# Optimization experiments

Hardware: AMD Instinct MI355X
Metric: run time of the kernel (lower is better)

The kernel has to match this reference:

```python
import jax, jax.numpy as jnp
import numpy as np
from jax import lax

EMB, HID, L, PATCH, IMG, K = 192, 64, 6, 4, 224, 8
FMAP = IMG // PATCH
N = FMAP * FMAP
B = 8
ALG = 4
GB_np = np.array([0, 1, 1, 2])  # grade of each blade [1, e1, e2, e12]
GB = jnp.asarray(GB_np)

def _cayley_np():
    C = np.zeros((4, 4, 4), np.float32)
    tbl = {(0,0):(0,1.),(0,1):(1,1.),(0,2):(2,1.),(0,3):(3,1.),
           (1,0):(1,1.),(1,1):(0,1.),(1,2):(3,1.),(1,3):(2,1.),
           (2,0):(2,1.),(2,1):(3,-1.),(2,2):(0,1.),(2,3):(1,-1.),
           (3,0):(3,1.),(3,1):(2,-1.),(3,2):(1,1.),(3,3):(0,-1.)}
    for (i, j), (k, s) in tbl.items():
        C[i, j, k] = s
    return C

CAY_np = _cayley_np()
CAYLEY = jnp.asarray(CAY_np)
_paths = np.zeros((3, 3, 3), bool)
for _i in range(4):
    for _j in range(4):
        for _k in range(4):
            if CAY_np[_i, _j, _k] != 0:
                _paths[GB_np[_i], GB_np[_j], GB_np[_k]] = True
PI, PJ, PK = (jnp.asarray(a) for a in np.nonzero(_paths))
NPATH = int(_paths.sum())  # 10 geometric-product paths for Cl(2,0)

def build_knn_graph(H, W, k):
    yy, xx = np.meshgrid(np.arange(H, dtype=np.float32), np.arange(W, dtype=np.float32), indexing='ij')
    coords = np.stack([xx.ravel(), yy.ravel()], -1)
    cn = coords / np.array([W - 1, H - 1], np.float32) * 2 - 1
    d = np.linalg.norm(cn[:, None] - cn[None], axis=-1)
    np.fill_diagonal(d, np.inf)
    idx = np.argsort(d, axis=-1, kind='stable')[:, :k]
    rows = np.repeat(np.arange(H * W), k)
    cols = idx.reshape(-1)
    return rows.astype(np.int32), cols.astype(np.int32), cn.astype(np.float32)

def mvlin(x, W, b=None):
    # per-grade MVLinear: W [out,in,3] expanded to blades via GB
    y = jnp.einsum('nmi,bmi->bni', W[:, :, GB], x)
    if b is not None:
        y = y.at[:, :, 0].add(b)  # bias embedded in scalar blade only
    return y

def mvlin_flat(x, W, b):
    # subspaces=False MVLinear: same weight across blades
    y = jnp.einsum('nm,bmi->bni', W, x)
    return y.at[:, :, 0].add(b)

def mv_silu(x, a, b):
    # invariants: [scalar, q(grade1), q(grade2)]; gate = sigmoid(a*inv+b)
    inv = jnp.concatenate([x[..., :1], x[..., 1:2]**2 + x[..., 2:3]**2, x[..., 3:4]**2], -1)
    return jax.nn.sigmoid(a * inv + b)[..., GB] * x

def normalize_mv(x, a):
    q = jnp.concatenate([x[..., :1]**2, x[..., 1:2]**2 + x[..., 2:3]**2, x[..., 3:4]**2], -1)
    n = jnp.sqrt(q + 1e-12)
    d = jax.nn.sigmoid(a) * (n - 1.0) + 1.0
    return x / (d + 1e-6)[..., GB]

def sgp(x, Wl, bl, Wr, na, gw):
    # SteerableGeometricProductLayer
    xr = normalize_mv(mvlin(x, Wr), na)
    full = jnp.zeros((gw.shape[0], 3, 3, 3), x.dtype).at[:, PI, PJ, PK].set(gw)
    fb = full[:, GB][:, :, GB][:, :, :, GB]  # [feat,4,4,4]
    gp = jnp.einsum('bni,nijk,bnk->bnj', x, CAYLEY[None] * fb, xr)
    return (mvlin(x, Wl, bl) + gp) * np.float32(1.0 / np.sqrt(2.0))

def _forward(x, conv_w, conv_b, stem_g, stem_b, pos_embed, in_W, in_b, in_Wl, in_bl, in_Wr, in_na, in_gw, eg_eW, eg_eb, eg_sa, eg_sb, eg_nW, eg_nb, eg_Wl, eg_bl, eg_Wr, eg_na, eg_gw, eg_aa, eg_ab, out_W, out_b, on_g, on_b, cls_W, cls_b, coords, rows, cols):
    Bx = x.shape[0]
    # stem: strided conv + LayerNorm over (C,H,W)
    y = lax.conv_general_dilated(x, conv_w, (PATCH, PATCH), 'VALID', dimension_numbers=('NCHW', 'OIHW', 'NCHW')) + conv_b[None, :, None, None]
    mu = y.mean(axis=(1, 2, 3), keepdims=True)
    var = ((y - mu) ** 2).mean(axis=(1, 2, 3), keepdims=True)
    y = (y - mu) / jnp.sqrt(var + 1e-5) * stem_g[None] + stem_b[None]
    y = y + pos_embed
    feat = y.transpose(0, 2, 3, 1).reshape(Bx * N, EMB)
    # embed features in scalar blade, coordinates in vector blades e1,e2
    h = jnp.zeros((Bx * N, EMB + 1, ALG), x.dtype)
    h = h.at[:, :EMB, 0].set(feat)
    h = h.at[:, EMB, 1:3].set(jnp.tile(coords, (Bx, 1)))
    h = sgp(mvlin_flat(h, in_W, in_b), in_Wl, in_bl, in_Wr, in_na, in_gw)
    BN = Bx * N
    for i in range(L):
        m = mv_silu(mvlin(h[rows] - h[cols], eg_eW[i], eg_eb[i]), eg_sa[i], eg_sb[i])
        agg = jax.ops.segment_sum(m, rows, num_segments=BN)  # count computed but unused in original
        nu = mvlin(jnp.concatenate([h, agg], axis=1), eg_nW[i], eg_nb[i])
        out = mv_silu(sgp(nu, eg_Wl[i], eg_bl[i], eg_Wr[i], eg_na[i], eg_gw[i]), eg_aa[i], eg_ab[i])
        h = h + out if i > 0 else out
    s = mvlin_flat(h, out_W, out_b)[..., 0]
    mu2 = s.mean(-1, keepdims=True)
    v2 = ((s - mu2) ** 2).mean(-1, keepdims=True)
    s = (s - mu2) / jnp.sqrt(v2 + 1e-5) * on_g + on_b
    pooled = s.reshape(Bx, N, EMB).mean(axis=1)
    return pooled @ cls_W.T + cls_b

def setup_inputs() -> dict:
    key = jax.random.key(0)
    ks = iter(jax.random.split(key, 64))
    nrm = lambda shape, s=0.05: jax.random.normal(next(ks), shape, jnp.float32) * s
    rows, cols, cn = build_knn_graph(FMAP, FMAP, K)
    offs = np.arange(B, dtype=np.int32)[:, None] * N
    rows_b = (rows[None] + offs).reshape(-1)
    cols_b = (cols[None] + offs).reshape(-1)
    return dict(
        x=jax.random.normal(next(ks), (B, 3, IMG, IMG), jnp.float32),
        conv_w=nrm((EMB, 3, PATCH, PATCH)),
        conv_b=jnp.zeros((EMB,), jnp.float32),
        stem_g=jnp.ones((EMB, FMAP, FMAP), jnp.float32),
        stem_b=jnp.zeros((EMB, FMAP, FMAP), jnp.float32),
        pos_embed=nrm((1, EMB, FMAP, FMAP), 0.02),
        coords=jnp.asarray(cn),
        in_W=nrm((HID, EMB + 1)), in_b=jnp.zeros((HID,), jnp.float32),
        in_Wl=nrm((HID, HID, 3)), in_bl=jnp.zeros((HID,), jnp.float32),
        in_Wr=nrm((HID, HID, 3)), in_na=jnp.zeros((HID, 3), jnp.float32),
        in_gw=nrm((HID, NPATH), 0.2),
        eg_eW=nrm((L, HID, HID, 3)), eg_eb=jnp.zeros((L, HID), jnp.float32),
        eg_sa=jnp.ones((L, HID, 3), jnp.float32), eg_sb=jnp.zeros((L, HID, 3), jnp.float32),
        eg_nW=nrm((L, HID, 2 * HID, 3)), eg_nb=jnp.zeros((L, HID), jnp.float32),
        eg_Wl=nrm((L, HID, HID, 3)), eg_bl=jnp.zeros((L, HID), jnp.float32),
        eg_Wr=nrm((L, HID, HID, 3)), eg_na=jnp.zeros((L, HID, 3), jnp.float32),
        eg_gw=nrm((L, HID, NPATH), 0.2),
        eg_aa=jnp.ones((L, HID, 3), jnp.float32), eg_ab=jnp.zeros((L, HID, 3), jnp.float32),
        out_W=nrm((EMB, HID)), out_b=jnp.zeros((EMB,), jnp.float32),
        on_g=jnp.ones((EMB,), jnp.float32), on_b=jnp.zeros((EMB,), jnp.float32),
        cls_W=nrm((10, EMB), 0.02), cls_b=jnp.zeros((10,), jnp.float32),
        rows=jnp.asarray(rows_b), cols=jnp.asarray(cols_b),
    )

def reference(x, conv_w, conv_b, stem_g, stem_b, pos_embed, coords, in_W, in_b, in_Wl, in_bl, in_Wr, in_na, in_gw, eg_eW, eg_eb, eg_sa, eg_sb, eg_nW, eg_nb, eg_Wl, eg_bl, eg_Wr, eg_na, eg_gw, eg_aa, eg_ab, out_W, out_b, on_g, on_b, cls_W, cls_b, rows, cols):
    return _forward(x, conv_w, conv_b, stem_g, stem_b, pos_embed, in_W, in_b, in_Wl, in_bl, in_Wr, in_na, in_gw, eg_eW, eg_eb, eg_sa, eg_sb, eg_nW, eg_nb, eg_Wl, eg_bl, eg_Wr, eg_na, eg_gw, eg_aa, eg_ab, out_W, out_b, on_g, on_b, cls_W, cls_b, coords, rows, cols)
```

## Files before the change

### kernel.cpp

```cpp
#include <hip/hip_runtime.h>
#include <hip/hip_bf16.h>
#include <math.h>

#define EMBC   192
#define NLAY   6
#define IMGC   224
#define FMAPC  56
#define NNODE  3136
#define NBATCH 8
#define BNODES 25088
#define KNNE   8
#define NT     64
#define RSQRT2 0.70710678118654752f

__device__ __forceinline__ float sigm(float x){ return 1.0f/(1.0f+__expf(-x)); }

__global__ void k_repackw(const float* __restrict__ src, float* __restrict__ dst, int K){
  int l = blockIdx.y;
  size_t S = (size_t)64*K*3;
  int t = blockIdx.x*256 + threadIdx.x;
  if(t < (int)S){
    int j = t % 3; int r = t / 3;
    int ci = r % 8; int m = (r / 8) % K; int wid = r / (8*K);
    dst[l*S + (((size_t)wid*K + m)*8 + ci)*3 + j] =
      src[l*S + ((size_t)(wid*8+ci)*K + m)*3 + j];
  }
}
__global__ void k_repack1(const float* __restrict__ src, float* __restrict__ dst,
                          int R, int K){
  int t = blockIdx.x*256 + threadIdx.x;
  if(t < R*K){
    int m = t % K, r = t / K;
    dst[m*R + r] = src[r*K + m];
  }
}

__global__ void k_tr(const float* __restrict__ g, const float* __restrict__ sb,
                     const float* __restrict__ pe, float* __restrict__ g2,
                     float* __restrict__ pb2){
  int n = blockIdx.x; int c = threadIdx.x;
  g2[n*EMBC + c]  = g[c*NNODE + n];
  pb2[n*EMBC + c] = sb[c*NNODE + n] + pe[c*NNODE + n];
}

__global__ __launch_bounds__(256) void k_conv(const float* __restrict__ x,
    const float* __restrict__ cw, const float* __restrict__ cb,
    float* __restrict__ y0, float* __restrict__ parts){
  __shared__ float xs[2688];
  __shared__ float wsh[9216];
  __shared__ float red[512];
  int blk = blockIdx.x; int b = blk / FMAPC; int ph = blk % FMAPC;
  int tid = threadIdx.x;
  for(int t = tid; t < 9216; t += 256) wsh[t] = cw[t];
  for(int t = tid; t < 2688; t += 256){
    int r = t / IMGC; int w = t % IMGC;
    int ci = r >> 2, kh = r & 3;
    xs[t] = x[((size_t)(b*3 + ci)*IMGC + (ph*4 + kh))*IMGC + w];
  }
  __syncthreads();
  float s1 = 0.f, s2 = 0.f;
  for(int oi = tid; oi < FMAPC*EMBC; oi += 256){
    int pw = oi / EMBC; int c = oi % EMBC;
    float acc = cb[c];
    const float4* wv4 = (const float4*)(wsh + c*48);
    #pragma unroll
    for(int r = 0; r < 12; ++r){
      float4 xv = *((const float4*)(xs + r*IMGC + pw*4));
      float4 wv = wv4[r];
      acc += xv.x*wv.x + xv.y*wv.y + xv.z*wv.z + xv.w*wv.w;
    }
    y0[((size_t)(b*NNODE + ph*FMAPC + pw))*EMBC + c] = acc;
    s1 += acc; s2 += acc*acc;
  }
  red[tid] = s1; red[256+tid] = s2;
  __syncthreads();
  for(int st = 128; st > 0; st >>= 1){
    if(tid < st){ red[tid] += red[tid+st]; red[256+tid] += red[256+tid+st]; }
    __syncthreads();
  }
  if(tid == 0){ parts[blk*2] = red[0]; parts[blk*2+1] = red[256]; }
}

__global__ void k_stats(const float* __restrict__ parts, float* __restrict__ stats){
  int b = threadIdx.x;
  if(b < NBATCH){
    float S = 0.f, Q = 0.f;
    for(int j = 0; j < FMAPC; ++j){ S += parts[(b*FMAPC+j)*2]; Q += parts[(b*FMAPC+j)*2+1]; }
    float cnt = (float)(EMBC*NNODE);
    float mu = S/cnt;
    float var = Q/cnt - mu*mu;
    stats[b*2] = mu; stats[b*2+1] = rsqrtf(var + 1e-5f);
  }
}

__global__ __launch_bounds__(256,2) void k_embed(const float* __restrict__ y0,
    const float* __restrict__ stats, const float* __restrict__ g2,
    const float* __restrict__ pb2, const float* __restrict__ inWp,
    const float* __restrict__ inb, const float* __restrict__ coords,
    float* __restrict__ xmv){
  __shared__ float fs[64*193];
  int tid = threadIdx.x, lane = tid & 63;
  int wid = __builtin_amdgcn_readfirstlane(tid >> 6);
  int ch0 = wid << 4;
  int p0 = blockIdx.x * 64;
  int b = p0 / NNODE; int n0 = p0 - b*NNODE;
  float mu = stats[b*2], rstd = stats[b*2+1];
  for(int t = tid; t < 64*192; t += 256){
    int n = t / 192, c = t - n*192;
    int nn = n0 + n;
    fs[n*193 + c] = (y0[(size_t)(p0+n)*192 + c] - mu)*rstd*g2[nn*192+c] + pb2[nn*192+c];
  }
  __syncthreads();
  float acc[16];
  #pragma unroll
  for(int ci = 0; ci < 16; ++ci) acc[ci] = 0.f;
  #pragma unroll 2
  for(int m = 0; m < 192; ++m){
    float xm = fs[lane*193 + m];
    const float* wp = inWp + m*64 + ch0;
    #pragma unroll
    for(int ci = 0; ci < 16; ++ci) acc[ci] += wp[ci]*xm;
  }
  float cx = coords[(n0+lane)*2], cy = coords[(n0+lane)*2+1];
  #pragma unroll
  for(int ci = 0; ci < 16; ++ci){
    int ch = ch0 + ci;
    float wc = inWp[192*64 + ch];
    float4 v; v.x = acc[ci] + inb[ch]; v.y = wc*cx; v.z = wc*cy; v.w = 0.f;
    *((float4*)(xmv + ((size_t)(p0+lane)*64 + ch)*4)) = v;
  }
}

__device__ __forceinline__ void stage_x(float* xs, const float* __restrict__ g,
                                        int p0, int tid){
  #pragma unroll
  for(int t = tid; t < NT*64; t += 512){
    int n = t >> 6, m = t & 63;
    *((float4*)(xs + (n<<8) + (((m + n)&63)<<2))) =
      *((const float4*)(g + (((size_t)(p0+n))<<8) + (m<<2)));
  }
}
__device__ __forceinline__ void copyout(const float* xs, float* __restrict__ g,
                                        int p0, int tid){
  #pragma unroll
  for(int t = tid; t < NT*64; t += 512){
    int n = t >> 6, m = t & 63;
    float4 v = *((const float4*)(xs + (n<<8) + (((m + n)&63)<<2)));
    *((float4*)(g + (((size_t)(p0+n))<<8) + (m<<2))) = v;
  }
}
__device__ __forceinline__ void stage_w(float* wst, const float* __restrict__ Wp,
                                        int K, int moff, int tid){
  #pragma unroll
  for(int t = tid; t < 3072; t += 512){
    int c = t / 384, r = t - c*384;
    ((float4*)wst)[t] = ((const float4*)(Wp + ((size_t)(c*K + moff)*24)))[r];
  }
}
__device__ __forceinline__ void mm2(float (&p)[4][4], float (&q)[4][4],
    const float* __restrict__ wst, const float* __restrict__ xr0,
    const float* __restrict__ xr1, int wb, int n){
  #pragma unroll 4
  for(int m = 0; m < 64; ++m){
    float4 x0 = *((const float4*)(xr0 + (((m + n)&63)<<2)));
    float4 x1 = *((const float4*)(xr1 + (((m + n + 32)&63)<<2)));
    const float* wp = wst + wb + m*24;
    float4 a = *((const float4*)wp);
    float4 b = *((const float4*)(wp+4));
    float4 c = *((const float4*)(wp+8));
    p[0][0]+=a.x*x0.x; p[0][1]+=a.y*x0.y; p[0][2]+=a.y*x0.z; p[0][3]+=a.z*x0.w;
    p[1][0]+=a.w*x0.x; p[1][1]+=b.x*x0.y; p[1][2]+=b.x*x0.z; p[1][3]+=b.y*x0.w;
    p[2][0]+=b.z*x0.x; p[2][1]+=b.w*x0.y; p[2][2]+=b.w*x0.z; p[2][3]+=c.x*x0.w;
    p[3][0]+=c.y*x0.x; p[3][1]+=c.z*x0.y; p[3][2]+=c.z*x0.z; p[3][3]+=c.w*x0.w;
    q[0][0]+=a.x*x1.x; q[0][1]+=a.y*x1.y; q[0][2]+=a.y*x1.z; q[0][3]+=a.z*x1.w;
    q[1][0]+=a.w*x1.x; q[1][1]+=b.x*x1.y; q[1][2]+=b.x*x1.z; q[1][3]+=b.y*x1.w;
    q[2][0]+=b.z*x1.x; q[2][1]+=b.w*x1.y; q[2][2]+=b.w*x1.z; q[2][3]+=c.x*x1.w;
    q[3][0]+=c.y*x1.x; q[3][1]+=c.z*x1.y; q[3][2]+=c.z*x1.z; q[3][3]+=c.w*x1.w;
  }
}
#define ZERO44(A) { _Pragma("unroll") for(int _i=0;_i<4;++_i) _Pragma("unroll") for(int _j=0;_j<4;++_j) A[_i][_j]=0.f; }

__global__ __launch_bounds__(512,1) void k_sgp0(const float* __restrict__ src,
    float* __restrict__ h, float* __restrict__ zout,
    const float* __restrict__ Wlp, const float* __restrict__ bl,
    const float* __restrict__ Wrp, const float* __restrict__ na,
    const float* __restrict__ gw, const float* __restrict__ zWp){
  __shared__ float xs[NT*256];
  __shared__ float wst[12288];
  int tid = threadIdx.x, lane = tid & 63;
  int wid = __builtin_amdgcn_readfirstlane(tid >> 6);
  int n = lane & 31, s = lane >> 5;
  int ch0 = (wid<<3) + s*4;
  int wb = wid*1536 + s*12;
  int p0 = blockIdx.x * NT;
  const float* xr0 = xs + (n<<8);
  const float* xr1 = xs + ((n+32)<<8);
  stage_x(xs, src, p0, tid);
  stage_w(wst, Wlp, 64, 0, tid);
  __syncthreads();
  float lA[4][4], lB[4][4], rA[4][4], rB[4][4];
  ZERO44(lA); ZERO44(lB); ZERO44(rA); ZERO44(rB);
  mm2(lA, lB, wst, xr0, xr1, wb, n);
  __syncthreads();
  stage_w(wst, Wrp, 64, 0, tid);
  __syncthreads();
  mm2(rA, rB, wst, xr0, xr1, wb, n);
  float oA[4][4], oB[4][4];
  #pragma unroll
  for(int j = 0; j < 2; ++j){
    int nn = n + j*32;
    #pragma unroll
    for(int ci = 0; ci < 4; ++ci){
      int ch = ch0 + ci;
      float yr0 = j? rB[ci][0]:rA[ci][0], yr1 = j? rB[ci][1]:rA[ci][1];
      float yr2 = j? rB[ci][2]:rA[ci][2], yr3 = j? rB[ci][3]:rA[ci][3];
      float na0 = sigm(na[ch*3]), na1 = sigm(na[ch*3+1]), na2 = sigm(na[ch*3+2]);
      float d0 = na0*(sqrtf(yr0*yr0 + 1e-12f) - 1.f) + 1.f + 1e-6f;
      float d1 = na1*(sqrtf(yr1*yr1 + yr2*yr2 + 1e-12f) - 1.f) + 1.f + 1e-6f;
      float d2 = na2*(sqrtf(yr3*yr3 + 1e-12f) - 1.f) + 1.f + 1e-6f;
      float xq0 = yr0/d0, xq1 = yr1/d1, xq2 = yr2/d1, xq3 = yr3/d2;
      float4 xv = *((const float4*)(xs + (nn<<8) + (((ch + nn)&63)<<2)));
      const float* gwp = gw + ch*10;
      float gp0 = gwp[0]*xv.x*xq0 + gwp[3]*(xv.y*xq1 + xv.z*xq2) + gwp[7]*xv.w*xq3;
      float gp1 = gwp[1]*xv.x*xq1 + gwp[4]*xv.y*xq0 - gwp[5]*xv.z*xq3 - gwp[8]*xv.w*xq2;
      float gp2 = gwp[1]*xv.x*xq2 + gwp[4]*xv.z*xq0 + gwp[5]*xv.y*xq3 + gwp[8]*xv.w*xq1;
      float gp3 = gwp[2]*xv.x*xq3 + gwp[6]*(xv.y*xq2 - xv.z*xq1) - gwp[9]*xv.w*xq0;
      float l0 = j? lB[ci][0]:lA[ci][0], l1 = j? lB[ci][1]:lA[ci][1];
      float l2 = j? lB[ci][2]:lA[ci][2], l3 = j? lB[ci][3]:lA[ci][3];
      float* o = j? oB[ci] : oA[ci];
      o[0] = (l0 + bl[ch] + gp0)*RSQRT2;
      o[1] = (l1 + gp1)*RSQRT2;
      o[2] = (l2 + gp2)*RSQRT2;
      o[3] = (l3 + gp3)*RSQRT2;
    }
  }
  __syncthreads();
  #pragma unroll
  for(int ci = 0; ci < 4; ++ci){
    int ch = ch0 + ci;
    float4 v0; v0.x=oA[ci][0]; v0.y=oA[ci][1]; v0.z=oA[ci][2]; v0.w=oA[ci][3];
    *((float4*)(xs + (n<<8) + (((ch + n)&63)<<2))) = v0;
    float4 v1; v1.x=oB[ci][0]; v1.y=oB[ci][1]; v1.z=oB[ci][2]; v1.w=oB[ci][3];
    *((float4*)(xs + ((n+32)<<8) + (((ch + n + 32)&63)<<2))) = v1;
  }
  __syncthreads();
  copyout(xs, h, p0, tid);
  stage_w(wst, zWp, 64, 0, tid);
  __syncthreads();
  float zA[4][4], zB[4][4];
  ZERO44(zA); ZERO44(zB);
  mm2(zA, zB, wst, xr0, xr1, wb, n);
  __syncthreads();
  #pragma unroll
  for(int ci = 0; ci < 4; ++ci){
    int ch = ch0 + ci;
    float4 v0; v0.x=zA[ci][0]; v0.y=zA[ci][1]; v0.z=zA[ci][2]; v0.w=zA[ci][3];
    *((float4*)(xs + (n<<8) + (((ch + n)&63)<<2))) = v0;
    float4 v1; v1.x=zB[ci][0]; v1.y=zB[ci][1]; v1.z=zB[ci][2]; v1.w=zB[ci][3];
    *((float4*)(xs + ((n+32)<<8) + (((ch + n + 32)&63)<<2))) = v1;
  }
  __syncthreads();
  copyout(xs, zout, p0, tid);
}

__global__ __launch_bounds__(512,1) void k_layer(
    float* __restrict__ h, const float* __restrict__ z,
    float* __restrict__ zout, const int* __restrict__ cols,
    const float* __restrict__ eb, const float* __restrict__ sa,
    const float* __restrict__ sb,
    const float* __restrict__ nWp, const float* __restrict__ nb,
    const float* __restrict__ Wlp, const float* __restrict__ bl,
    const float* __restrict__ Wrp, const float* __restrict__ na,
    const float* __restrict__ gw, const float* __restrict__ aa,
    const float* __restrict__ ab,
    const float* __restrict__ zWp, int mode){
  __shared__ float xs[NT*256];
  __shared__ float wst[12288];
  int tid = threadIdx.x, lane = tid & 63;
  int wid = __builtin_amdgcn_readfirstlane(tid >> 6);
  int n = lane & 31, s = lane >> 5;
  int ch0 = (wid<<3) + s*4;
  int wb = wid*1536 + s*12;
  int p0 = blockIdx.x * NT;
  const float* xr0 = xs + (n<<8);
  const float* xr1 = xs + ((n+32)<<8);
  float ag[8][4];
  {
    int ch = lane;
    float ebv = eb[ch];
    float a0 = sa[ch*3], a1 = sa[ch*3+1], a2 = sa[ch*3+2];
    float b0 = sb[ch*3], b1 = sb[ch*3+1], b2 = sb[ch*3+2];
    #pragma unroll
    for(int e = 0; e < 8; ++e){
      int p = p0 + wid*8 + e;
      float4 zo = *((const float4*)(z + ((size_t)p*64 + ch)*4));
      float ax=0.f, ay=0.f, az_=0.f, aw=0.f;
      #pragma unroll
      for(int k = 0; k < KNNE; ++k){
        int c = cols[p*KNNE + k];
        float4 zc = *((const float4*)(z + ((size_t)c*64 + ch)*4));
        float d0 = zo.x - zc.x + ebv;
        float d1 = zo.y - zc.y;
        float d2 = zo.z - zc.z;
        float d3 = zo.w - zc.w;
        float g0 = sigm(a0*d0 + b0);
        float g1 = sigm(a1*(d1*d1 + d2*d2) + b1);
        float g2v = sigm(a2*(d3*d3) + b2);
        ax += g0*d0; ay += g1*d1; az_ += g1*d2; aw += g2v*d3;
      }
      ag[e][0]=ax; ag[e][1]=ay; ag[e][2]=az_; ag[e][3]=aw;
    }
  }
  stage_x(xs, h, p0, tid);
  stage_w(wst, nWp, 128, 0, tid);
  __syncthreads();
  float nuA[4][4], nuB[4][4];
  ZERO44(nuA); ZERO44(nuB);
  mm2(nuA, nuB, wst, xr0, xr1, wb, n);
  float hrA[4][4], hrB[4][4];
  if(mode == 2){
    #pragma unroll
    for(int ci = 0; ci < 4; ++ci){
      int ch = ch0 + ci;
      float4 v0 = *((const float4*)(xr0 + (((ch + n)&63)<<2)));
      float4 v1 = *((const float4*)(xr1 + (((ch + n + 32)&63)<<2)));
      hrA[ci][0]=v0.x; hrA[ci][1]=v0.y; hrA[ci][2]=v0.z; hrA[ci][3]=v0.w;
      hrB[ci][0]=v1.x; hrB[ci][1]=v1.y; hrB[ci][2]=v1.z; hrB[ci][3]=v1.w;
    }
  }
  __syncthreads();
  #pragma unroll
  for(int e = 0; e < 8; ++e){
    int nn = wid*8 + e;
    float4 v; v.x=ag[e][0]; v.y=ag[e][1]; v.z=ag[e][2]; v.w=ag[e][3];
    *((float4*)(xs + (nn<<8) + (((lane + nn)&63)<<2))) = v;
  }
  stage_w(wst, nWp, 128, 64, tid);
  __syncthreads();
  mm2(nuA, nuB, wst, xr0, xr1, wb, n);
  __syncthreads();
  #pragma unroll
  for(int ci = 0; ci < 4; ++ci){
    int ch = ch0 + ci;
    nuA[ci][0] += nb[ch]; nuB[ci][0] += nb[ch];
    float4 v0; v0.x=nuA[ci][0]; v0.y=nuA[ci][1]; v0.z=nuA[ci][2]; v0.w=nuA[ci][3];
    *((float4*)(xs + (n<<8) + (((ch + n)&63)<<2))) = v0;
    float4 v1; v1.x=nuB[ci][0]; v1.y=nuB[ci][1]; v1.z=nuB[ci][2]; v1.w=nuB[ci][3];
    *((float4*)(xs + ((n+32)<<8) + (((ch + n + 32)&63)<<2))) = v1;
  }
  stage_w(wst, Wlp, 64, 0, tid);
  __syncthreads();
  float lA[4][4], lB[4][4];
  ZERO44(lA); ZERO44(lB);
  mm2(lA, lB, wst, xr0, xr1, wb, n);
  __syncthreads();
  stage_w(wst, Wrp, 64, 0, tid);
  __syncthreads();
  float rA[4][4], rB[4][4];
  ZERO44(rA); ZERO44(rB);
  mm2(rA, rB, wst, xr0, xr1, wb, n);
  float oA[4][4], oB[4][4];
  #pragma unroll
  for(int j = 0; j < 2; ++j){
    #pragma unroll
    for(int ci = 0; ci < 4; ++ci){
      int ch = ch0 + ci;
      float yr0 = j? rB[ci][0]:rA[ci][0], yr1 = j? rB[ci][1]:rA[ci][1];
      float yr2 = j? rB[ci][2]:rA[ci][2], yr3 = j? rB[ci][3]:rA[ci][3];
      float na0 = sigm(na[ch*3]), na1 = sigm(na[ch*3+1]), na2 = sigm(na[ch*3+2]);
      float d0 = na0*(sqrtf(yr0*yr0 + 1e-12f) - 1.f) + 1.f + 1e-6f;
      float d1 = na1*(sqrtf(yr1*yr1 + yr2*yr2 + 1e-12f) - 1.f) + 1.f + 1e-6f;
      float d2 = na2*(sqrtf(yr3*yr3 + 1e-12f) - 1.f) + 1.f + 1e-6f;
      float xq0 = yr0/d0, xq1 = yr1/d1, xq2 = yr2/d1, xq3 = yr3/d2;
      float x0 = j? nuB[ci][0]:nuA[ci][0], x1 = j? nuB[ci][1]:nuA[ci][1];
      float x2 = j? nuB[ci][2]:nuA[ci][2], x3 = j? nuB[ci][3]:nuA[ci][3];
      const float* gwp = gw + ch*10;
      float gp0 = gwp[0]*x0*xq0 + gwp[3]*(x1*xq1 + x2*xq2) + gwp[7]*x3*xq3;
      float gp1 = gwp[1]*x0*xq1 + gwp[4]*x1*xq0 - gwp[5]*x2*xq3 - gwp[8]*x3*xq2;
      float gp2 = gwp[1]*x0*xq2 + gwp[4]*x2*xq0 + gwp[5]*x1*xq3 + gwp[8]*x3*xq1;
      float gp3 = gwp[2]*x0*xq3 + gwp[6]*(x1*xq2 - x2*xq1) - gwp[9]*x3*xq0;
      float l0 = j? lB[ci][0]:lA[ci][0], l1 = j? lB[ci][1]:lA[ci][1];
      float l2 = j? lB[ci][2]:lA[ci][2], l3 = j? lB[ci][3]:lA[ci][3];
      float o0 = (l0 + bl[ch] + gp0)*RSQRT2;
      float o1 = (l1 + gp1)*RSQRT2;
      float o2 = (l2 + gp2)*RSQRT2;
      float o3 = (l3 + gp3)*RSQRT2;
      float g0 = sigm(aa[ch*3]*o0 + ab[ch*3]);
      float g1 = sigm(aa[ch*3+1]*(o1*o1 + o2*o2) + ab[ch*3+1]);
      float g2v = sigm(aa[ch*3+2]*(o3*o3) + ab[ch*3+2]);
      float v0 = g0*o0, v1 = g1*o1, v2 = g1*o2, v3 = g2v*o3;
      if(mode == 2){
        if(j){ v0 += hrB[ci][0]; v1 += hrB[ci][1]; v2 += hrB[ci][2]; v3 += hrB[ci][3]; }
        else { v0 += hrA[ci][0]; v1 += hrA[ci][1]; v2 += hrA[ci][2]; v3 += hrA[ci][3]; }
      }
      float* o = j? oB[ci] : oA[ci];
      o[0]=v0; o[1]=v1; o[2]=v2; o[3]=v3;
    }
  }
  __syncthreads();
  #pragma unroll
  for(int ci = 0; ci < 4; ++ci){
    int ch = ch0 + ci;
    float4 v0; v0.x=oA[ci][0]; v0.y=oA[ci][1]; v0.z=oA[ci][2]; v0.w=oA[ci][3];
    *((float4*)(xs + (n<<8) + (((ch + n)&63)<<2))) = v0;
    float4 v1; v1.x=oB[ci][0]; v1.y=oB[ci][1]; v1.z=oB[ci][2]; v1.w=oB[ci][3];
    *((float4*)(xs + ((n+32)<<8) + (((ch + n + 32)&63)<<2))) = v1;
  }
  __syncthreads();
  copyout(xs, h, p0, tid);
  if(zWp != nullptr){
    stage_w(wst, zWp, 64, 0, tid);
    __syncthreads();
    float zA[4][4], zB[4][4];
    ZERO44(zA); ZERO44(zB);
    mm2(zA, zB, wst, xr0, xr1, wb, n);
    __syncthreads();
    #pragma unroll
    for(int ci = 0; ci < 4; ++ci){
      int ch = ch0 + ci;
      float4 v0; v0.x=zA[ci][0]; v0.y=zA[ci][1]; v0.z=zA[ci][2]; v0.w=zA[ci][3];
      *((float4*)(xs + (n<<8) + (((ch + n)&63)<<2))) = v0;
      float4 v1; v1.x=zB[ci][0]; v1.y=zB[ci][1]; v1.z=zB[ci][2]; v1.w=zB[ci][3];
      *((float4*)(xs + ((n+32)<<8) + (((ch + n + 32)&63)<<2))) = v1;
    }
    __syncthreads();
    copyout(xs, zout, p0, tid);
  }
}

__global__ __launch_bounds__(256,2) void k_head(const float* __restrict__ h,
    const float* __restrict__ oWp, const float* __restrict__ ob,
    const float* __restrict__ ong, const float* __restrict__ onb,
    float* __restrict__ s){
  __shared__ float hs[64*65];
  __shared__ float rr[512];
  int tid = threadIdx.x, lane = tid & 63;
  int wid = __builtin_amdgcn_readfirstlane(tid >> 6);
  int c0 = wid*48;
  int p0 = blockIdx.x * 64;
  for(int t = tid; t < 64*64; t += 256){
    int nn = t >> 6, c = t & 63;
    hs[nn*65 + c] = h[(((size_t)(p0+nn))*64 + c)*4];
  }
  __syncthreads();
  float a[48];
  #pragma unroll
  for(int ci = 0; ci < 48; ++ci) a[ci] = 0.f;
  #pragma unroll 2
  for(int m = 0; m < 64; ++m){
    float xm = hs[lane*65 + m];
    const float* wp = oWp + m*192 + c0;
    #pragma unroll
    for(int ci = 0; ci < 48; ++ci) a[ci] += wp[ci]*xm;
  }
  float s1 = 0.f, s2 = 0.f;
  #pragma unroll
  for(int ci = 0; ci < 48; ++ci){
    a[ci] += ob[c0+ci];
    s1 += a[ci]; s2 += a[ci]*a[ci];
  }
  rr[wid*64 + lane] = s1; rr[256 + wid*64 + lane] = s2;
  __syncthreads();
  float S = rr[lane] + rr[64+lane] + rr[128+lane] + rr[192+lane];
  float Q = rr[256+lane] + rr[320+lane] + rr[384+lane] + rr[448+lane];
  float mu = S*(1.0f/EMBC);
  float var = Q*(1.0f/EMBC) - mu*mu;
  float rstd = rsqrtf(var + 1e-5f);
  #pragma unroll
  for(int q = 0; q < 12; ++q){
    int c = c0 + q*4;
    float4 v;
    v.x = (a[q*4  ] - mu)*rstd*ong[c  ] + onb[c  ];
    v.y = (a[q*4+1] - mu)*rstd*ong[c+1] + onb[c+1];
    v.z = (a[q*4+2] - mu)*rstd*ong[c+2] + onb[c+2];
    v.w = (a[q*4+3] - mu)*rstd*ong[c+3] + onb[c+3];
    *((float4*)(s + (size_t)(p0+lane)*192 + c)) = v;
  }
}

__global__ void k_pool1(const float* __restrict__ s, float* __restrict__ pp){
  int blk = blockIdx.x;
  int b = blk >> 5, chunk = blk & 31;
  int c = threadIdx.x;
  float acc = 0.f;
  int n0 = chunk*98;
  for(int j = 0; j < 98; ++j) acc += s[((size_t)(b*NNODE + n0 + j))*EMBC + c];
  pp[(size_t)blk*EMBC + c] = acc;
}
__global__ void k_pool2(const float* __restrict__ pp, float* __restrict__ pooled){
  int b = blockIdx.x; int c = threadIdx.x;
  float acc = 0.f;
  for(int j = 0; j < 32; ++j) acc += pp[((size_t)(b*32 + j))*EMBC + c];
  pooled[b*EMBC + c] = acc * (1.0f/NNODE);
}

__global__ void k_cls(const float* __restrict__ pooled, const float* __restrict__ cW,
                      const float* __restrict__ cb, float* __restrict__ out){
  int tid = threadIdx.x;
  if(tid < NBATCH*10){
    int b = tid/10, k = tid%10;
    float acc = cb[k];
    for(int c = 0; c < EMBC; ++c) acc += pooled[b*EMBC + c]*cW[k*EMBC + c];
    out[tid] = acc;
  }
}

extern "C" void kernel_launch(void* const* d_in, const int* in_sizes, int n_in,
                              void* d_out, int out_size, void* d_ws, size_t ws_size,
                              hipStream_t stream){
  const float* x      = (const float*)d_in[0];
  const float* conv_w = (const float*)d_in[1];
  const float* conv_b = (const float*)d_in[2];
  const float* stem_g = (const float*)d_in[3];
  const float* stem_b = (const float*)d_in[4];
  const float* pos_e  = (const float*)d_in[5];
  const float* coords = (const float*)d_in[6];
  const float* inW    = (const float*)d_in[7];
  const float* inb    = (const float*)d_in[8];
  const float* inWl   = (const float*)d_in[9];
  const float* inbl   = (const float*)d_in[10];
  const float* inWr   = (const float*)d_in[11];
  const float* inna   = (const float*)d_in[12];
  const float* ingw   = (const float*)d_in[13];
  const float* eg_eW  = (const float*)d_in[14];
  const float* eg_eb  = (const float*)d_in[15];
  const float* eg_sa  = (const float*)d_in[16];
  const float* eg_sb  = (const float*)d_in[17];
  const float* eg_nW  = (const float*)d_in[18];
  const float* eg_nb  = (const float*)d_in[19];
  const float* eg_Wl  = (const float*)d_in[20];
  const float* eg_bl  = (const float*)d_in[21];
  const float* eg_Wr  = (const float*)d_in[22];
  const float* eg_na  = (const float*)d_in[23];
  const float* eg_gw  = (const float*)d_in[24];
  const float* eg_aa  = (const float*)d_in[25];
  const float* eg_ab  = (const float*)d_in[26];
  const float* outW   = (const float*)d_in[27];
  const float* outb   = (const float*)d_in[28];
  const float* ong    = (const float*)d_in[29];
  const float* onb    = (const float*)d_in[30];
  const float* clsW   = (const float*)d_in[31];
  const float* clsb   = (const float*)d_in[32];
  const int*   cols   = (const int*)d_in[34];

  float* ws = (float*)d_ws;
  size_t off = 0;
  float* hbuf  = ws + off; off += (size_t)BNODES*256;
  float* bigA  = ws + off; off += (size_t)BNODES*256;
  float* bigB  = ws + off; off += (size_t)BNODES*256;
  float* g2    = ws + off; off += (size_t)NNODE*EMBC;
  float* pb2   = ws + off; off += (size_t)NNODE*EMBC;
  float* parts = ws + off; off += 896;
  float* stats = ws + off; off += 16;
  float* pp    = ws + off; off += 256*EMBC;
  float* pooled= ws + off; off += NBATCH*EMBC;
  float* wpInW = ws + off; off += 193*64;
  float* wpOW  = ws + off; off += 64*192;
  float* wpInWl= ws + off; off += 12288;
  float* wpInWr= ws + off; off += 12288;
  float* wpEW  = ws + off; off += (size_t)NLAY*12288;
  float* wpWl  = ws + off; off += (size_t)NLAY*12288;
  float* wpWr  = ws + off; off += (size_t)NLAY*12288;
  float* wpNW  = ws + off; off += (size_t)NLAY*24576;
  float* y0    = bigB;

  const int NTILE = BNODES/NT;

  { dim3 g1((12352+255)/256); k_repack1<<<g1, 256, 0, stream>>>(inW,  wpInW, 64, 193); }
  { dim3 g1((12288+255)/256); k_repack1<<<g1, 256, 0, stream>>>(outW, wpOW, 192, 64); }
  { dim3 g3((12288+255)/256, 1); k_repackw<<<g3, 256, 0, stream>>>(inWl, wpInWl, 64); }
  { dim3 g3((12288+255)/256, 1); k_repackw<<<g3, 256, 0, stream>>>(inWr, wpInWr, 64); }
  { dim3 g3((12288+255)/256, NLAY); k_repackw<<<g3, 256, 0, stream>>>(eg_eW, wpEW, 64); }
  { dim3 g3((12288+255)/256, NLAY); k_repackw<<<g3, 256, 0, stream>>>(eg_Wl, wpWl, 64); }
  { dim3 g3((12288+255)/256, NLAY); k_repackw<<<g3, 256, 0, stream>>>(eg_Wr, wpWr, 64); }
  { dim3 g3((24576+255)/256, NLAY); k_repackw<<<g3, 256, 0, stream>>>(eg_nW, wpNW, 128); }

  k_tr   <<<NNODE, 192, 0, stream>>>(stem_g, stem_b, pos_e, g2, pb2);
  k_conv <<<NBATCH*FMAPC, 256, 0, stream>>>(x, conv_w, conv_b, y0, parts);
  k_stats<<<1, 64, 0, stream>>>(parts, stats);
  k_embed<<<BNODES/64, 256, 0, stream>>>(y0, stats, g2, pb2, wpInW, inb, coords, bigA);
  k_sgp0 <<<NTILE, 512, 0, stream>>>(bigA, hbuf, bigB, wpInWl, inbl, wpInWr,
                                     inna, ingw, wpEW);
  float* zcur = bigB;
  float* spare = bigA;
  for(int l = 0; l < NLAY; ++l){
    const float* zWn = (l < NLAY-1) ? (wpEW + (size_t)(l+1)*12288) : (const float*)nullptr;
    k_layer<<<NTILE, 512, 0, stream>>>(hbuf, zcur, spare, cols,
        eg_eb + l*64, eg_sa + l*192, eg_sb + l*192,
        wpNW + (size_t)l*24576, eg_nb + l*64,
        wpWl + (size_t)l*12288, eg_bl + l*64,
        wpWr + (size_t)l*12288, eg_na + l*192,
        eg_gw + l*640, eg_aa + l*192, eg_ab + l*192,
        zWn, (l==0)?1:2);
    if(l < NLAY-1){ float* t = zcur; zcur = spare; spare = t; }
  }
  k_head <<<BNODES/64, 256, 0, stream>>>(hbuf, wpOW, outb, ong, onb, spare);
  k_pool1<<<256, 192, 0, stream>>>(spare, pp);
  k_pool2<<<8, 192, 0, stream>>>(pp, pooled);
  k_cls  <<<1, 128, 0, stream>>>(pooled, clsW, clsb, (float*)d_out);
}
```

Before: 1.637 ms.

## Halve node tile to 32 with 256-thread blocks and XCD-aware block swizzle

Shrinks the per-block node tile from 64 to 32 and the block from 512 to 256 threads, so each wave now covers 16 channels across 16 node pairs. The weight repack and staging layout change to 16 channels per wave to match, and launch bounds allow two blocks per CU. Block indices in the embed, layer and head kernels are remapped so neighbouring tiles go to the same XCD, aiming for better L2 locality on the kNN gathers. The trade-off is that each weight tile staged into shared memory is reused across half as many nodes.

```diff
diff --git a/kernel.cpp b/kernel.cpp
--- a/kernel.cpp
+++ b/kernel.cpp
@@ -10,7 +10,7 @@
 #define NBATCH 8
 #define BNODES 25088
 #define KNNE   8
-#define NT     64
+#define NT     32
 #define RSQRT2 0.70710678118654752f
 
 __device__ __forceinline__ float sigm(float x){ return 1.0f/(1.0f+__expf(-x)); }
@@ -21,9 +21,9 @@
   int t = blockIdx.x*256 + threadIdx.x;
   if(t < (int)S){
     int j = t % 3; int r = t / 3;
-    int ci = r % 8; int m = (r / 8) % K; int wid = r / (8*K);
-    dst[l*S + (((size_t)wid*K + m)*8 + ci)*3 + j] =
-      src[l*S + ((size_t)(wid*8+ci)*K + m)*3 + j];
+    int cw = r % 16; int m = (r / 16) % K; int widx = r / (16*K);
+    dst[l*S + (((size_t)widx*K + m)*16 + cw)*3 + j] =
+      src[l*S + ((size_t)(widx*16+cw)*K + m)*3 + j];
   }
 }
 __global__ void k_repack1(const float* __restrict__ src, float* __restrict__ dst,
@@ -102,7 +102,9 @@
   int tid = threadIdx.x, lane = tid & 63;
   int wid = __builtin_amdgcn_readfirstlane(tid >> 6);
   int ch0 = wid << 4;
-  int p0 = blockIdx.x * 64;
+  int bid = blockIdx.x;
+  int blk = (bid & 7)*49 + (bid >> 3);
+  int p0 = blk * 64;
   int b = p0 / NNODE; int n0 = p0 - b*NNODE;
   float mu = stats[b*2], rstd = stats[b*2+1];
   for(int t = tid; t < 64*192; t += 256){
@@ -134,7 +136,7 @@
 __device__ __forceinline__ void stage_x(float* xs, const float* __restrict__ g,
                                         int p0, int tid){
   #pragma unroll
-  for(int t = tid; t < NT*64; t += 512){
+  for(int t = tid; t < NT*64; t += 256){
     int n = t >> 6, m = t & 63;
     *((float4*)(xs + (n<<8) + (((m + n)&63)<<2))) =
       *((const float4*)(g + (((size_t)(p0+n))<<8) + (m<<2)));
@@ -143,7 +145,7 @@
 __device__ __forceinline__ void copyout(const float* xs, float* __restrict__ g,
                                         int p0, int tid){
   #pragma unroll
-  for(int t = tid; t < NT*64; t += 512){
+  for(int t = tid; t < NT*64; t += 256){
     int n = t >> 6, m = t & 63;
     float4 v = *((const float4*)(xs + (n<<8) + (((m + n)&63)<<2)));
     *((float4*)(g + (((size_t)(p0+n))<<8) + (m<<2))) = v;
@@ -152,35 +154,35 @@
 __device__ __forceinline__ void stage_w(float* wst, const float* __restrict__ Wp,
                                         int K, int moff, int tid){
   #pragma unroll
-  for(int t = tid; t < 3072; t += 512){
-    int c = t / 384, r = t - c*384;
-    ((float4*)wst)[t] = ((const float4*)(Wp + ((size_t)(c*K + moff)*24)))[r];
-  }
-}
-__device__ __forceinline__ void mm2(float (&p)[4][4], float (&q)[4][4],
-    const float* __restrict__ wst, const float* __restrict__ xr0,
-    const float* __restrict__ xr1, int wb, int n){
+  for(int t = tid; t < 3072; t += 256){
+    int c = t / 768, r = t - c*768;
+    ((float4*)wst)[t] = ((const float4*)(Wp + ((size_t)(c*K + moff)*48)))[r];
+  }
+}
+__device__ __forceinline__ void mm2n(float (&pA)[4][4], float (&pB)[4][4],
+    const float* __restrict__ wst, const float* __restrict__ xrA,
+    const float* __restrict__ xrB, int wb, int np){
   #pragma unroll 4
   for(int m = 0; m < 64; ++m){
-    float4 x0 = *((const float4*)(xr0 + (((m + n)&63)<<2)));
-    float4 x1 = *((const float4*)(xr1 + (((m + n + 32)&63)<<2)));
-    const float* wp = wst + wb + m*24;
+    float4 xa = *((const float4*)(xrA + (((m + np)&63)<<2)));
+    float4 xb = *((const float4*)(xrB + (((m + np + 16)&63)<<2)));
+    const float* wp = wst + wb + m*48;
     float4 a = *((const float4*)wp);
     float4 b = *((const float4*)(wp+4));
     float4 c = *((const float4*)(wp+8));
-    p[0][0]+=a.x*x0.x; p[0][1]+=a.y*x0.y; p[0][2]+=a.y*x0.z; p[0][3]+=a.z*x0.w;
-    p[1][0]+=a.w*x0.x; p[1][1]+=b.x*x0.y; p[1][2]+=b.x*x0.z; p[1][3]+=b.y*x0.w;
-    p[2][0]+=b.z*x0.x; p[2][1]+=b.w*x0.y; p[2][2]+=b.w*x0.z; p[2][3]+=c.x*x0.w;
-    p[3][0]+=c.y*x0.x; p[3][1]+=c.z*x0.y; p[3][2]+=c.z*x0.z; p[3][3]+=c.w*x0.w;
-    q[0][0]+=a.x*x1.x; q[0][1]+=a.y*x1.y; q[0][2]+=a.y*x1.z; q[0][3]+=a.z*x1.w;
-    q[1][0]+=a.w*x1.x; q[1][1]+=b.x*x1.y; q[1][2]+=b.x*x1.z; q[1][3]+=b.y*x1.w;
-    q[2][0]+=b.z*x1.x; q[2][1]+=b.w*x1.y; q[2][2]+=b.w*x1.z; q[2][3]+=c.x*x1.w;
-    q[3][0]+=c.y*x1.x; q[3][1]+=c.z*x1.y; q[3][2]+=c.z*x1.z; q[3][3]+=c.w*x1.w;
+    pA[0][0]+=a.x*xa.x; pA[0][1]+=a.y*xa.y; pA[0][2]+=a.y*xa.z; pA[0][3]+=a.z*xa.w;
+    pA[1][0]+=a.w*xa.x; pA[1][1]+=b.x*xa.y; pA[1][2]+=b.x*xa.z; pA[1][3]+=b.y*xa.w;
+    pA[2][0]+=b.z*xa.x; pA[2][1]+=b.w*xa.y; pA[2][2]+=b.w*xa.z; pA[2][3]+=c.x*xa.w;
+    pA[3][0]+=c.y*xa.x; pA[3][1]+=c.z*xa.y; pA[3][2]+=c.z*xa.z; pA[3][3]+=c.w*xa.w;
+    pB[0][0]+=a.x*xb.x; pB[0][1]+=a.y*xb.y; pB[0][2]+=a.y*xb.z; pB[0][3]+=a.z*xb.w;
+    pB[1][0]+=a.w*xb.x; pB[1][1]+=b.x*xb.y; pB[1][2]+=b.x*xb.z; pB[1][3]+=b.y*xb.w;
+    pB[2][0]+=b.z*xb.x; pB[2][1]+=b.w*xb.y; pB[2][2]+=b.w*xb.z; pB[2][3]+=c.x*xb.w;
+    pB[3][0]+=c.y*xb.x; pB[3][1]+=c.z*xb.y; pB[3][2]+=c.z*xb.z; pB[3][3]+=c.w*xb.w;
   }
 }
 #define ZERO44(A) { _Pragma("unroll") for(int _i=0;_i<4;++_i) _Pragma("unroll") for(int _j=0;_j<4;++_j) A[_i][_j]=0.f; }
 
-__global__ __launch_bounds__(512,1) void k_sgp0(const float* __restrict__ src,
+__global__ __launch_bounds__(256,2) void k_sgp0(const float* __restrict__ src,
     float* __restrict__ h, float* __restrict__ zout,
     const float* __restrict__ Wlp, const float* __restrict__ bl,
     const float* __restrict__ Wrp, const float* __restrict__ na,
@@ -188,27 +190,31 @@
   __shared__ float xs[NT*256];
   __shared__ float wst[12288];
   int tid = threadIdx.x, lane = tid & 63;
-  int wid = __builtin_amdgcn_readfirstlane(tid >> 6);
-  int n = lane & 31, s = lane >> 5;
-  int ch0 = (wid<<3) + s*4;
-  int wb = wid*1536 + s*12;
-  int p0 = blockIdx.x * NT;
-  const float* xr0 = xs + (n<<8);
-  const float* xr1 = xs + ((n+32)<<8);
+  int widx = __builtin_amdgcn_readfirstlane(tid >> 6);
+  int np = lane & 15, qw = lane >> 4;
+  int ch0 = widx*16 + qw*4;
+  int wb = widx*3072 + qw*12;
+  int bid = blockIdx.x;
+  int blk = (bid & 7)*98 + (bid >> 3);
+  int p0 = blk * NT;
+  const float* xrA = xs + (np<<8);
+  const float* xrB = xs + ((np+16)<<8);
   stage_x(xs, src, p0, tid);
   stage_w(wst, Wlp, 64, 0, tid);
   __syncthreads();
-  float lA[4][4], lB[4][4], rA[4][4], rB[4][4];
-  ZERO44(lA); ZERO44(lB); ZERO44(rA); ZERO44(rB);
-  mm2(lA, lB, wst, xr0, xr1, wb, n);
+  float lA[4][4], lB[4][4];
+  ZERO44(lA); ZERO44(lB);
+  mm2n(lA, lB, wst, xrA, xrB, wb, np);
   __syncthreads();
   stage_w(wst, Wrp, 64, 0, tid);
   __syncthreads();
-  mm2(rA, rB, wst, xr0, xr1, wb, n);
+  float rA[4][4], rB[4][4];
+  ZERO44(rA); ZERO44(rB);
+  mm2n(rA, rB, wst, xrA, xrB, wb, np);
   float oA[4][4], oB[4][4];
   #pragma unroll
   for(int j = 0; j < 2; ++j){
-    int nn = n + j*32;
+    int nn = np + j*16;
     #pragma unroll
     for(int ci = 0; ci < 4; ++ci){
       int ch = ch0 + ci;
@@ -239,9 +245,9 @@
   for(int ci = 0; ci < 4; ++ci){
     int ch = ch0 + ci;
     float4 v0; v0.x=oA[ci][0]; v0.y=oA[ci][1]; v0.z=oA[ci][2]; v0.w=oA[ci][3];
-    *((float4*)(xs + (n<<8) + (((ch + n)&63)<<2))) = v0;
+    *((float4*)(xs + (np<<8) + (((ch + np)&63)<<2))) = v0;
     float4 v1; v1.x=oB[ci][0]; v1.y=oB[ci][1]; v1.z=oB[ci][2]; v1.w=oB[ci][3];
-    *((float4*)(xs + ((n+32)<<8) + (((ch + n + 32)&63)<<2))) = v1;
+    *((float4*)(xs + ((np+16)<<8) + (((ch + np + 16)&63)<<2))) = v1;
   }
   __syncthreads();
   copyout(xs, h, p0, tid);
@@ -249,21 +255,21 @@
   __syncthreads();
   float zA[4][4], zB[4][4];
   ZERO44(zA); ZERO44(zB);
-  mm2(zA, zB, wst, xr0, xr1, wb, n);
+  mm2n(zA, zB, wst, xrA, xrB, wb, np);
   __syncthreads();
   #pragma unroll
   for(int ci = 0; ci < 4; ++ci){
     int ch = ch0 + ci;
     float4 v0; v0.x=zA[ci][0]; v0.y=zA[ci][1]; v0.z=zA[ci][2]; v0.w=zA[ci][3];
-    *((float4*)(xs + (n<<8) + (((ch + n)&63)<<2))) = v0;
+    *((float4*)(xs + (np<<8) + (((ch + np)&63)<<2))) = v0;
     float4 v1; v1.x=zB[ci][0]; v1.y=zB[ci][1]; v1.z=zB[ci][2]; v1.w=zB[ci][3];
-    *((float4*)(xs + ((n+32)<<8) + (((ch + n + 32)&63)<<2))) = v1;
+    *((float4*)(xs + ((np+16)<<8) + (((ch + np + 16)&63)<<2))) = v1;
   }
   __syncthreads();
   copyout(xs, zout, p0, tid);
 }
 
-__global__ __launch_bounds__(512,1) void k_layer(
+__global__ __launch_bounds__(256,2) void k_layer(
     float* __restrict__ h, const float* __restrict__ z,
     float* __restrict__ zout, const int* __restrict__ cols,
     const float* __restrict__ eb, const float* __restrict__ sa,
@@ -277,13 +283,15 @@
   __shared__ float xs[NT*256];
   __shared__ float wst[12288];
   int tid = threadIdx.x, lane = tid & 63;
-  int wid = __builtin_amdgcn_readfirstlane(tid >> 6);
-  int n = lane & 31, s = lane >> 5;
-  int ch0 = (wid<<3) + s*4;
-  int wb = wid*1536 + s*12;
-  int p0 = blockIdx.x * NT;
-  const float* xr0 = xs + (n<<8);
-  const float* xr1 = xs + ((n+32)<<8);
+  int widx = __builtin_amdgcn_readfirstlane(tid >> 6);
+  int np = lane & 15, qw = lane >> 4;
+  int ch0 = widx*16 + qw*4;
+  int wb = widx*3072 + qw*12;
+  int bid = blockIdx.x;
+  int blk = (bid & 7)*98 + (bid >> 3);
+  int p0 = blk * NT;
+  const float* xrA = xs + (np<<8);
+  const float* xrB = xs + ((np+16)<<8);
   float ag[8][4];
   {
     int ch = lane;
@@ -292,7 +300,7 @@
     float b0 = sb[ch*3], b1 = sb[ch*3+1], b2 = sb[ch*3+2];
     #pragma unroll
     for(int e = 0; e < 8; ++e){
-      int p = p0 + wid*8 + e;
+      int p = p0 + widx*8 + e;
       float4 zo = *((const float4*)(z + ((size_t)p*64 + ch)*4));
       float ax=0.f, ay=0.f, az_=0.f, aw=0.f;
       #pragma unroll
@@ -316,14 +324,14 @@
   __syncthreads();
   float nuA[4][4], nuB[4][4];
   ZERO44(nuA); ZERO44(nuB);
-  mm2(nuA, nuB, wst, xr0, xr1, wb, n);
+  mm2n(nuA, nuB, wst, xrA, xrB, wb, np);
   float hrA[4][4], hrB[4][4];
   if(mode == 2){
     #pragma unroll
     for(int ci = 0; ci < 4; ++ci){
       int ch = ch0 + ci;
-      float4 v0 = *((const float4*)(xr0 + (((ch + n)&63)<<2)));
-      float4 v1 = *((const float4*)(xr1 + (((ch + n + 32)&63)<<2)));
+      float4 v0 = *((const float4*)(xrA + (((ch + np)&63)<<2)));
+      float4 v1 = *((const float4*)(xrB + (((ch + np + 16)&63)<<2)));
       hrA[ci][0]=v0.x; hrA[ci][1]=v0.y; hrA[ci][2]=v0.z; hrA[ci][3]=v0.w;
       hrB[ci][0]=v1.x; hrB[ci][1]=v1.y; hrB[ci][2]=v1.z; hrB[ci][3]=v1.w;
     }
@@ -331,34 +339,34 @@
   __syncthreads();
   #pragma unroll
   for(int e = 0; e < 8; ++e){
-    int nn = wid*8 + e;
+    int nn = widx*8 + e;
     float4 v; v.x=ag[e][0]; v.y=ag[e][1]; v.z=ag[e][2]; v.w=ag[e][3];
     *((float4*)(xs + (nn<<8) + (((lane + nn)&63)<<2))) = v;
   }
   stage_w(wst, nWp, 128, 64, tid);
   __syncthreads();
-  mm2(nuA, nuB, wst, xr0, xr1, wb, n);
+  mm2n(nuA, nuB, wst, xrA, xrB, wb, np);
   __syncthreads();
   #pragma unroll
   for(int ci = 0; ci < 4; ++ci){
     int ch = ch0 + ci;
     nuA[ci][0] += nb[ch]; nuB[ci][0] += nb[ch];
     float4 v0; v0.x=nuA[ci][0]; v0.y=nuA[ci][1]; v0.z=nuA[ci][2]; v0.w=nuA[ci][3];
-    *((float4*)(xs + (n<<8) + (((ch + n)&63)<<2))) = v0;
+    *((float4*)(xs + (np<<8) + (((ch + np)&63)<<2))) = v0;
     float4 v1; v1.x=nuB[ci][0]; v1.y=nuB[ci][1]; v1.z=nuB[ci][2]; v1.w=nuB[ci][3];
-    *((float4*)(xs + ((n+32)<<8) + (((ch + n + 32)&63)<<2))) = v1;
+    *((float4*)(xs + ((np+16)<<8) + (((ch + np + 16)&63)<<2))) = v1;
   }
   stage_w(wst, Wlp, 64, 0, tid);
   __syncthreads();
   float lA[4][4], lB[4][4];
   ZERO44(lA); ZERO44(lB);
-  mm2(lA, lB, wst, xr0, xr1, wb, n);
+  mm2n(lA, lB, wst, xrA, xrB, wb, np);
   __syncthreads();
   stage_w(wst, Wrp, 64, 0, tid);
   __syncthreads();
   float rA[4][4], rB[4][4];
   ZERO44(rA); ZERO44(rB);
-  mm2(rA, rB, wst, xr0, xr1, wb, n);
+  mm2n(rA, rB, wst, xrA, xrB, wb, np);
   float oA[4][4], oB[4][4];
   #pragma unroll
   for(int j = 0; j < 2; ++j){
@@ -402,9 +410,9 @@
   for(int ci = 0; ci < 4; ++ci){
     int ch = ch0 + ci;
     float4 v0; v0.x=oA[ci][0]; v0.y=oA[ci][1]; v0.z=oA[ci][2]; v0.w=oA[ci][3];
-    *((float4*)(xs + (n<<8) + (((ch + n)&63)<<2))) = v0;
+    *((float4*)(xs + (np<<8) + (((ch + np)&63)<<2))) = v0;
     float4 v1; v1.x=oB[ci][0]; v1.y=oB[ci][1]; v1.z=oB[ci][2]; v1.w=oB[ci][3];
-    *((float4*)(xs + ((n+32)<<8) + (((ch + n + 32)&63)<<2))) = v1;
+    *((float4*)(xs + ((np+16)<<8) + (((ch + np + 16)&63)<<2))) = v1;
   }
   __syncthreads();
   copyout(xs, h, p0, tid);
@@ -413,15 +421,15 @@
     __syncthreads();
     float zA[4][4], zB[4][4];
     ZERO44(zA); ZERO44(zB);
-    mm2(zA, zB, wst, xr0, xr1, wb, n);
+    mm2n(zA, zB, wst, xrA, xrB, wb, np);
     __syncthreads();
     #pragma unroll
     for(int ci = 0; ci < 4; ++ci){
       int ch = ch0 + ci;
       float4 v0; v0.x=zA[ci][0]; v0.y=zA[ci][1]; v0.z=zA[ci][2]; v0.w=zA[ci][3];
-      *((float4*)(xs + (n<<8) + (((ch + n)&63)<<2))) = v0;
+      *((float4*)(xs + (np<<8) + (((ch + np)&63)<<2))) = v0;
       float4 v1; v1.x=zB[ci][0]; v1.y=zB[ci][1]; v1.z=zB[ci][2]; v1.w=zB[ci][3];
-      *((float4*)(xs + ((n+32)<<8) + (((ch + n + 32)&63)<<2))) = v1;
+      *((float4*)(xs + ((np+16)<<8) + (((ch + np + 16)&63)<<2))) = v1;
     }
     __syncthreads();
     copyout(xs, zout, p0, tid);
@@ -437,7 +445,9 @@
   int tid = threadIdx.x, lane = tid & 63;
   int wid = __builtin_amdgcn_readfirstlane(tid >> 6);
   int c0 = wid*48;
-  int p0 = blockIdx.x * 64;
+  int bid = blockIdx.x;
+  int blk = (bid & 7)*49 + (bid >> 3);
+  int p0 = blk * 64;
   for(int t = tid; t < 64*64; t += 256){
     int nn = t >> 6, c = t & 63;
     hs[nn*65 + c] = h[(((size_t)(p0+nn))*64 + c)*4];
@@ -579,13 +589,13 @@
   k_conv <<<NBATCH*FMAPC, 256, 0, stream>>>(x, conv_w, conv_b, y0, parts);
   k_stats<<<1, 64, 0, stream>>>(parts, stats);
   k_embed<<<BNODES/64, 256, 0, stream>>>(y0, stats, g2, pb2, wpInW, inb, coords, bigA);
-  k_sgp0 <<<NTILE, 512, 0, stream>>>(bigA, hbuf, bigB, wpInWl, inbl, wpInWr,
+  k_sgp0 <<<NTILE, 256, 0, stream>>>(bigA, hbuf, bigB, wpInWl, inbl, wpInWr,
                                      inna, ingw, wpEW);
   float* zcur = bigB;
   float* spare = bigA;
   for(int l = 0; l < NLAY; ++l){
     const float* zWn = (l < NLAY-1) ? (wpEW + (size_t)(l+1)*12288) : (const float*)nullptr;
-    k_layer<<<NTILE, 512, 0, stream>>>(hbuf, zcur, spare, cols,
+    k_layer<<<NTILE, 256, 0, stream>>>(hbuf, zcur, spare, cols,
         eg_eb + l*64, eg_sa + l*192, eg_sb + l*192,
         wpNW + (size_t)l*24576, eg_nb + l*64,
         wpWl + (size_t)l*12288, eg_bl + l*64,
```

Result: faster. 1.493 ms (-8.8%).
